# Kernel tuning notes

Hardware: AMD Instinct MI355X
Metric: run time of the kernel (lower is better)

The kernel has to match this reference:

```python
import jax, jax.numpy as jnp
import numpy as np

B, S, H = 2, 2048, 2048
NH, NKV, D = 32, 8, 64
GROUPS = NH // NKV
SCALE = D ** -0.5


def rotate_half(x):
    x1, x2 = x[..., : D // 2], x[..., D // 2 :]
    return jnp.concatenate((-x2, x1), axis=-1)


def setup_inputs() -> dict:
    key = jax.random.key(0)
    ks = jax.random.split(key, 8)
    x = jax.random.normal(ks[0], (B, S, H), dtype=jnp.float32)
    cos = jax.random.uniform(ks[1], (B, S, D), dtype=jnp.float32)
    sin = jax.random.uniform(ks[2], (B, S, D), dtype=jnp.float32)
    mask = jnp.tril(jnp.ones((S, S), dtype=jnp.int32))[None, None]  # causal (1,1,S,S)
    std = H ** -0.5
    wq = jax.random.normal(ks[3], (NH * D, H), dtype=jnp.float32) * std
    wk = jax.random.normal(ks[4], (NKV * D, H), dtype=jnp.float32) * std
    wv = jax.random.normal(ks[5], (NKV * D, H), dtype=jnp.float32) * std
    wo = jax.random.normal(ks[6], (H, NH * D), dtype=jnp.float32) * std
    return {"x": x, "cos": cos, "sin": sin, "mask": mask,
            "wq": wq, "wk": wk, "wv": wv, "wo": wo}


def reference(x, cos, sin, mask, wq, wk, wv, wo):
    b, s, _ = x.shape
    # projections (Linear: x @ W^T, no bias)
    q = (x @ wq.T).reshape(b, s, NH, D).transpose(0, 2, 1, 3)    # (b, nh, s, d)
    k = (x @ wk.T).reshape(b, s, NKV, D).transpose(0, 2, 1, 3)   # (b, nkv, s, d)
    v = (x @ wv.T).reshape(b, s, NKV, D).transpose(0, 2, 1, 3)
    # RoPE
    c = cos[:, None, :, :]
    sn = sin[:, None, :, :]
    q = q * c + rotate_half(q) * sn
    k = k * c + rotate_half(k) * sn
    # GQA: repeat KV heads
    k = jnp.repeat(k, GROUPS, axis=1)   # (b, nh, s, d)
    v = jnp.repeat(v, GROUPS, axis=1)
    scores = jnp.einsum("bhqd,bhkd->bhqk", q, k) * SCALE
    scores = jnp.where(mask == 0, -jnp.inf, scores)
    weights = jax.nn.softmax(scores, axis=-1)
    out = jnp.einsum("bhqk,bhkd->bhqd", weights, v)
    out = out.transpose(0, 2, 1, 3).reshape(b, s, NH * D)
    return out @ wo.T
```

## Files before the change

kernel.cpp:

```cpp
#include <hip/hip_runtime.h>
#include <hip/hip_bf16.h>
#include <math.h>

typedef __attribute__((ext_vector_type(8))) short bf16x8;
typedef __attribute__((ext_vector_type(4))) float f32x4;

__device__ __forceinline__ float bf2f(ushort u) {
  union { unsigned u; float f; } v; v.u = ((unsigned)u) << 16; return v.f;
}
__device__ __forceinline__ ushort f2bf(float f) {
  union { float f; unsigned u; } v; v.f = f;
  unsigned r = v.u + 0x7FFFu + ((v.u >> 16) & 1u);
  return (ushort)(r >> 16);
}
#if __has_builtin(__builtin_amdgcn_exp2f)
#define EXP2F(x) __builtin_amdgcn_exp2f(x)
#else
#define EXP2F(x) exp2f(x)
#endif
__device__ __forceinline__ void gl_lds16(const ushort* g, ushort* l) {
  __builtin_amdgcn_global_load_lds(
      (const __attribute__((address_space(1))) unsigned int*)g,
      (__attribute__((address_space(3))) unsigned int*)l, 16, 0, 0);
}

static const long XB   = 0;
static const long WQB  = 8388608;
static const long WKB  = 12582912;
static const long WVB  = 13631488;
static const long WOB  = 14680064;
static const long COSB = 18874368;
static const long SINB = 19136512;
static const long QB   = 19398656;
static const long KB   = 27787264;
static const long VTB  = 29884416;

__global__ void detect_dtype(const ushort* __restrict__ x, int* __restrict__ flag) {
  __shared__ int cnt;
  if (threadIdx.x == 0) cnt = 0;
  __syncthreads();
  int local = 0;
  for (int j = 0; j < 32; j++) {
    ushort u = x[threadIdx.x + j * 256];
    int e = (u >> 7) & 0xFF;
    if (e >= 100 && e <= 142) local++;
  }
  atomicAdd(&cnt, local);
  __syncthreads();
  if (threadIdx.x == 0) *flag = (cnt >= 6554) ? 1 : 0;
}

__global__ void cast_all(const void* __restrict__ s0, const void* __restrict__ s1,
                         const void* __restrict__ s2, const void* __restrict__ s3,
                         const void* __restrict__ s4, const void* __restrict__ s5,
                         const void* __restrict__ s6,
                         ushort* __restrict__ d0, ushort* __restrict__ d1,
                         ushort* __restrict__ d2, ushort* __restrict__ d3,
                         ushort* __restrict__ d4, ushort* __restrict__ d5,
                         ushort* __restrict__ d6, const int* __restrict__ flag) {
  if (*flag) return;
  const long N = 2424832;
  for (long i = (long)blockIdx.x * blockDim.x + threadIdx.x; i < N;
       i += (long)gridDim.x * blockDim.x) {
    const float4* s; ushort* d; long off;
    if      (i < 1048576) { s = (const float4*)s0; d = d0; off = i; }
    else if (i < 1572864) { s = (const float4*)s1; d = d1; off = i - 1048576; }
    else if (i < 1703936) { s = (const float4*)s2; d = d2; off = i - 1572864; }
    else if (i < 1835008) { s = (const float4*)s3; d = d3; off = i - 1703936; }
    else if (i < 2359296) { s = (const float4*)s4; d = d4; off = i - 1835008; }
    else if (i < 2392064) { s = (const float4*)s5; d = d5; off = i - 2359296; }
    else                  { s = (const float4*)s6; d = d6; off = i - 2392064; }
    float4 a = s[2 * off], b = s[2 * off + 1];
    uint4 o;
    o.x = (unsigned)f2bf(a.x) | ((unsigned)f2bf(a.y) << 16);
    o.y = (unsigned)f2bf(a.z) | ((unsigned)f2bf(a.w) << 16);
    o.z = (unsigned)f2bf(b.x) | ((unsigned)f2bf(b.y) << 16);
    o.w = (unsigned)f2bf(b.z) | ((unsigned)f2bf(b.w) << 16);
    ((uint4*)d)[off] = o;
  }
}

__device__ __forceinline__ void gemm_body(
    const ushort* __restrict__ A, const ushort* __restrict__ W, void* __restrict__ C,
    int N, int K, int bm, int bn, bool ofp32, ushort* As, ushort* Ws) {
  const int tid = threadIdx.x;
  const int wave = tid >> 6, lane = tid & 63;
  const int quad = lane >> 4, l15 = lane & 15;
  const int wm = (wave >> 1) * 64, wn = (wave & 1) * 64;
  const int srow = tid >> 2, sk = (tid & 3) * 8;
  const ushort* Ap = A + (size_t)(bm + srow) * K + sk;
  const ushort* Wp = W + (size_t)(bn + srow) * K + sk;
  ushort* AsW = As + wave * 512;
  ushort* WsW = Ws + wave * 512;
  f32x4 acc[4][4] = {};
  for (int k0 = 0; k0 < K; k0 += 32) {
    __syncthreads();
    gl_lds16(Ap + k0, AsW);
    gl_lds16(Ap + (size_t)64 * K + k0, AsW + 2048);
    gl_lds16(Wp + k0, WsW);
    gl_lds16(Wp + (size_t)64 * K + k0, WsW + 2048);
    __syncthreads();
    bf16x8 af[4], wf[4];
#pragma unroll
    for (int t = 0; t < 4; t++)
      af[t] = *(const bf16x8*)&As[(wm + t * 16 + l15) * 32 + quad * 8];
#pragma unroll
    for (int t = 0; t < 4; t++)
      wf[t] = *(const bf16x8*)&Ws[(wn + t * 16 + l15) * 32 + quad * 8];
#pragma unroll
    for (int mt = 0; mt < 4; mt++)
#pragma unroll
      for (int nt = 0; nt < 4; nt++)
        acc[mt][nt] = __builtin_amdgcn_mfma_f32_16x16x32_bf16(af[mt], wf[nt], acc[mt][nt], 0, 0, 0);
  }
  if (!ofp32) {
    ushort* Cb = (ushort*)C;
#pragma unroll
    for (int mt = 0; mt < 4; mt++)
#pragma unroll
      for (int nt = 0; nt < 4; nt++)
#pragma unroll
        for (int r = 0; r < 4; r++) {
          int row = bm + wm + mt * 16 + quad * 4 + r;
          int col = bn + wn + nt * 16 + l15;
          Cb[(size_t)row * N + col] = f2bf(acc[mt][nt][r]);
        }
  } else {
    float* Cf = (float*)C;
#pragma unroll
    for (int mt = 0; mt < 4; mt++)
#pragma unroll
      for (int nt = 0; nt < 4; nt++)
#pragma unroll
        for (int r = 0; r < 4; r++) {
          int row = bm + wm + mt * 16 + quad * 4 + r;
          int col = bn + wn + nt * 16 + l15;
          Cf[(size_t)row * N + col] = acc[mt][nt][r];
        }
  }
}

__global__ __launch_bounds__(256) void gemm_qkv(
    const ushort* __restrict__ xws, const ushort* __restrict__ xorig,
    const ushort* __restrict__ wqws, const ushort* __restrict__ wqorig,
    const ushort* __restrict__ wkws, const ushort* __restrict__ wkorig,
    const ushort* __restrict__ wvws, const ushort* __restrict__ wvorig,
    ushort* __restrict__ qout, ushort* __restrict__ kout, ushort* __restrict__ vtout,
    const int* __restrict__ flag) {
  __shared__ __align__(16) ushort As[128 * 32];
  __shared__ __align__(16) ushort Ws[128 * 32];
  const bool bf = (*flag != 0);
  const ushort* x = bf ? xorig : xws;
  const int id = blockIdx.x;
  if (id < 512) {
    gemm_body(x, bf ? wqorig : wqws, qout, 2048, 2048, (id >> 4) * 128, (id & 15) * 128, false, As, Ws);
  } else if (id < 640) {
    int t = id - 512;
    gemm_body(x, bf ? wkorig : wkws, kout, 512, 2048, (t >> 2) * 128, (t & 3) * 128, false, As, Ws);
  } else {
    int t = id - 640;
    gemm_body(bf ? wvorig : wvws, x, vtout, 4096, 2048, (t & 3) * 128, (t >> 2) * 128, false, As, Ws);
  }
}

__global__ __launch_bounds__(256) void gemm_bt(
    const ushort* __restrict__ Aws, const ushort* __restrict__ Aorig,
    const ushort* __restrict__ Wws, const ushort* __restrict__ Worig,
    void* __restrict__ C, int N, int K, const int* __restrict__ flag, int outMode) {
  __shared__ __align__(16) ushort As[128 * 32];
  __shared__ __align__(16) ushort Ws[128 * 32];
  const bool bf = (*flag != 0);
  const ushort* A = (bf && Aorig) ? Aorig : Aws;
  const ushort* W = (bf && Worig) ? Worig : Wws;
  bool ofp32 = (outMode == 1) && !bf;
  gemm_body(A, W, C, N, K, blockIdx.y * 128, blockIdx.x * 128, ofp32, As, Ws);
}

__global__ void rope_kernel(ushort* __restrict__ Qb, ushort* __restrict__ Kb,
                            const ushort* __restrict__ cws, const ushort* __restrict__ corig,
                            const ushort* __restrict__ sws, const ushort* __restrict__ sorig,
                            const int* __restrict__ flag) {
  const ushort* cb = (*flag) ? corig : cws;
  const ushort* sb = (*flag) ? sorig : sws;
  int i = blockIdx.x * 256 + threadIdx.x;
  ushort* base; long row; int c8; float scl;
  if (i < 524288) {
    row = i >> 7; int rest = i & 127; c8 = (rest & 3) * 8;
    base = Qb + row * 2048 + (rest >> 2) * 64 + c8;
    scl = 0.18033688011112f;
  } else {
    int j = i - 524288;
    row = j >> 5; int rest = j & 31; c8 = (rest & 3) * 8;
    base = Kb + row * 512 + (rest >> 2) * 64 + c8;
    scl = 1.0f;
  }
  uint4 lo4 = *(const uint4*)base;
  uint4 hi4 = *(const uint4*)(base + 32);
  uint4 cl4 = *(const uint4*)(cb + row * 64 + c8);
  uint4 ch4 = *(const uint4*)(cb + row * 64 + c8 + 32);
  uint4 sl4 = *(const uint4*)(sb + row * 64 + c8);
  uint4 sh4 = *(const uint4*)(sb + row * 64 + c8 + 32);
  const ushort* lo = (const ushort*)&lo4; const ushort* hi = (const ushort*)&hi4;
  const ushort* cl = (const ushort*)&cl4; const ushort* ch = (const ushort*)&ch4;
  const ushort* sl = (const ushort*)&sl4; const ushort* sh = (const ushort*)&sh4;
  uint4 olo, ohi;
  ushort* po = (ushort*)&olo; ushort* ph = (ushort*)&ohi;
#pragma unroll
  for (int k = 0; k < 8; k++) {
    float l = bf2f(lo[k]), h = bf2f(hi[k]);
    po[k] = f2bf((l * bf2f(cl[k]) - h * bf2f(sl[k])) * scl);
    ph[k] = f2bf((h * bf2f(ch[k]) + l * bf2f(sh[k])) * scl);
  }
  *(uint4*)base = olo;
  *(uint4*)(base + 32) = ohi;
}

__global__ __launch_bounds__(512, 4) void attn_kernel(
    const ushort* __restrict__ Qb, const ushort* __restrict__ Kb,
    const ushort* __restrict__ Vt, ushort* __restrict__ Ob) {
  __shared__ __align__(16) ushort Ks[2][4096];
  __shared__ __align__(16) ushort Vs[2][4096];
  __shared__ __align__(16) ushort Ps[128 * 72];
  const int tid = threadIdx.x;
  const int wave = tid >> 6, lane = tid & 63;
  const int quad = lane >> 4, l15 = lane & 15;
  const int id = blockIdx.x;
  const int kvh = id & 7;
  const int b = (id >> 3) & 1;
  const int hsub = (id >> 4) & 3;
  const int h = kvh * 4 + hsub;
  const int pr = id >> 6;
  const size_t brow = (size_t)b * 2048;
  const ushort* Kg = Kb + brow * 512 + (size_t)kvh * 64;
  const ushort* Vg = Vt + (size_t)(kvh * 64) * 4096 + brow;

  const int prow = wave * 16 + (lane >> 2);
  const int chunk = (lane & 3) * 8;
  const int k_s = prow & 63, k_kc = prow >> 6;
  const int v_d = prow & 63, v_sc = prow >> 6;
  const int ldsW = wave * 512;

  for (int ph = 0; ph < 2; ph++) {
    const int t = ph ? (15 - pr) : pr;
    const int q0 = t * 128;
    const int wrow0 = q0 + wave * 16;
    const int blockNt = 2 * t + 2;
    const int myLast = wrow0 >> 6;

    gl_lds16(Kg + (size_t)k_s * 512 + k_kc * 32 + chunk, &Ks[0][ldsW]);
    gl_lds16(Vg + (size_t)v_d * 4096 + v_sc * 32 + chunk, &Vs[0][ldsW]);

    bf16x8 qf[2];
#pragma unroll
    for (int kc = 0; kc < 2; kc++)
      qf[kc] = *(const bf16x8*)&Qb[(brow + wrow0 + l15) * 2048 + h * 64 + kc * 32 + quad * 8];

    float l_s[4] = {};
    f32x4 oacc[4] = {};

    __syncthreads();

    for (int nt = 0; nt < blockNt; nt++) {
      const int cur = nt & 1;
      if (nt + 1 < blockNt) {
        const int n1 = (nt + 1) * 64;
        gl_lds16(Kg + (size_t)(n1 + k_s) * 512 + k_kc * 32 + chunk, &Ks[cur ^ 1][ldsW]);
        gl_lds16(Vg + (size_t)v_d * 4096 + n1 + v_sc * 32 + chunk, &Vs[cur ^ 1][ldsW]);
      }
      if (nt <= myLast) {
        const int n0 = nt * 64;
        const ushort* Kc = Ks[cur];
        const ushort* Vc = Vs[cur];
        f32x4 sc[4];
        __builtin_amdgcn_s_setprio(1);
#pragma unroll
        for (int ct = 0; ct < 4; ct++) {
          bf16x8 kf0 = *(const bf16x8*)&Kc[(ct * 16 + l15) * 32 + quad * 8];
          bf16x8 kf1 = *(const bf16x8*)&Kc[2048 + (ct * 16 + l15) * 32 + quad * 8];
          f32x4 z = {0.f, 0.f, 0.f, 0.f};
          z = __builtin_amdgcn_mfma_f32_16x16x32_bf16(qf[0], kf0, z, 0, 0, 0);
          z = __builtin_amdgcn_mfma_f32_16x16x32_bf16(qf[1], kf1, z, 0, 0, 0);
          sc[ct] = z;
        }
        __builtin_amdgcn_s_setprio(0);
        const int rowb = wrow0 + quad * 4;
        if (nt == myLast) {
#pragma unroll
          for (int ct = 0; ct < 4; ct++)
#pragma unroll
            for (int r = 0; r < 4; r++)
              if (n0 + ct * 16 + l15 > rowb + r) sc[ct][r] = -INFINITY;
        }
#pragma unroll
        for (int ct = 0; ct < 4; ct++)
#pragma unroll
          for (int r = 0; r < 4; r++) {
            float pv = EXP2F(sc[ct][r] - 23.083120654223f);
            l_s[r] += pv;
            Ps[(wave * 16 + quad * 4 + r) * 72 + ct * 16 + l15] =
                (ushort)((__float_as_uint(pv) + 0x8000u) >> 16);
          }
        bf16x8 pf0 = *(const bf16x8*)&Ps[(wave * 16 + l15) * 72 + quad * 8];
        bf16x8 pf1 = *(const bf16x8*)&Ps[(wave * 16 + l15) * 72 + 32 + quad * 8];
        __builtin_amdgcn_s_setprio(1);
#pragma unroll
        for (int dt = 0; dt < 4; dt++) {
          bf16x8 vf0 = *(const bf16x8*)&Vc[(dt * 16 + l15) * 32 + quad * 8];
          bf16x8 vf1 = *(const bf16x8*)&Vc[2048 + (dt * 16 + l15) * 32 + quad * 8];
          oacc[dt] = __builtin_amdgcn_mfma_f32_16x16x32_bf16(pf0, vf0, oacc[dt], 0, 0, 0);
          oacc[dt] = __builtin_amdgcn_mfma_f32_16x16x32_bf16(pf1, vf1, oacc[dt], 0, 0, 0);
        }
        __builtin_amdgcn_s_setprio(0);
      }
      __syncthreads();
    }
#pragma unroll
    for (int r = 0; r < 4; r++) {
      float l = l_s[r];
#pragma unroll
      for (int off = 1; off < 16; off <<= 1) l += __shfl_xor(l, off, 64);
      l_s[r] = 1.f / l;
    }
#pragma unroll
    for (int dt = 0; dt < 4; dt++)
#pragma unroll
      for (int r = 0; r < 4; r++) {
        int s = wrow0 + quad * 4 + r;
        Ob[(brow + s) * 2048 + h * 64 + dt * 16 + l15] = f2bf(oacc[dt][r] * l_s[r]);
      }
  }
}

extern "C" void kernel_launch(void* const* d_in, const int* in_sizes, int n_in,
                              void* d_out, int out_size, void* d_ws, size_t ws_size,
                              hipStream_t stream) {
  char* wsb = (char*)d_ws;
  int* flag = (int*)wsb;
  ushort* base = (ushort*)(wsb + 256);
  ushort* xb   = base + XB;
  ushort* wqb  = base + WQB;
  ushort* wkb  = base + WKB;
  ushort* wvb  = base + WVB;
  ushort* wob  = base + WOB;
  ushort* cosb = base + COSB;
  ushort* sinb = base + SINB;
  ushort* qb   = base + QB;
  ushort* kb   = base + KB;
  ushort* vtb  = base + VTB;
  ushort* abuf = xb;

  const ushort* xo  = (const ushort*)d_in[0];
  const ushort* co  = (const ushort*)d_in[1];
  const ushort* so  = (const ushort*)d_in[2];
  const ushort* wqo = (const ushort*)d_in[4];
  const ushort* wko = (const ushort*)d_in[5];
  const ushort* wvo = (const ushort*)d_in[6];
  const ushort* woo = (const ushort*)d_in[7];

  detect_dtype<<<1, 256, 0, stream>>>(xo, flag);

  cast_all<<<4096, 256, 0, stream>>>(d_in[0], d_in[4], d_in[5], d_in[6], d_in[7],
                                     d_in[1], d_in[2],
                                     xb, wqb, wkb, wvb, wob, cosb, sinb, flag);

  gemm_qkv<<<768, 256, 0, stream>>>(xb, xo, wqb, wqo, wkb, wko, wvb, wvo,
                                    qb, kb, vtb, flag);

  rope_kernel<<<2560, 256, 0, stream>>>(qb, kb, cosb, co, sinb, so, flag);

  attn_kernel<<<512, 512, 0, stream>>>(qb, kb, vtb, abuf);

  gemm_bt<<<dim3(16, 32), 256, 0, stream>>>(abuf, nullptr, wob, woo, d_out, 2048, 2048, flag, 1);
}
```

Before: 317.3 us.

## Fuse RoPE into QKV GEMM epilogue and split attention into one tile per block

RoPE is now applied in the QKV GEMM epilogue, pairing accumulator columns nt and nt^2 inside each 64-wide head tile, so the separate rope kernel and its extra read-modify-write pass over Q and K go away. The attention kernel stops looping over two paired query tiles per block. It launches 1024 blocks, each handling one tile, largest first. The QK MFMA operands are swapped so scores come out transposed, which lets P be written to LDS as packed 32-bit pairs and the row sum be reduced with fewer shuffles. The epilogue now does strided cos/sin loads, and per-block causal work is no longer balanced by pairing tiles.

```diff
diff --git a/kernel.cpp b/kernel.cpp
--- a/kernel.cpp
+++ b/kernel.cpp
@@ -82,7 +82,8 @@
 
 __device__ __forceinline__ void gemm_body(
     const ushort* __restrict__ A, const ushort* __restrict__ W, void* __restrict__ C,
-    int N, int K, int bm, int bn, bool ofp32, ushort* As, ushort* Ws) {
+    int N, int K, int bm, int bn, bool ofp32, ushort* As, ushort* Ws,
+    int ropeMode, const ushort* __restrict__ cosp, const ushort* __restrict__ sinp) {
   const int tid = threadIdx.x;
   const int wave = tid >> 6, lane = tid & 63;
   const int quad = lane >> 4, l15 = lane & 15;
@@ -113,7 +114,28 @@
       for (int nt = 0; nt < 4; nt++)
         acc[mt][nt] = __builtin_amdgcn_mfma_f32_16x16x32_bf16(af[mt], wf[nt], acc[mt][nt], 0, 0, 0);
   }
-  if (!ofp32) {
+  if (ropeMode) {
+    ushort* Cb = (ushort*)C;
+    const float scl = (ropeMode == 1) ? 0.18033688011112f : 1.0f;
+#pragma unroll
+    for (int mt = 0; mt < 4; mt++)
+#pragma unroll
+      for (int r = 0; r < 4; r++) {
+        int row = bm + wm + mt * 16 + quad * 4 + r;
+        const ushort* crow = cosp + (size_t)row * 64;
+        const ushort* srw  = sinp + (size_t)row * 64;
+#pragma unroll
+        for (int nt = 0; nt < 4; nt++) {
+          int d = nt * 16 + l15;
+          float a = acc[mt][nt][r];
+          float p = acc[mt][nt ^ 2][r];
+          float cs = bf2f(crow[d]), sn = bf2f(srw[d]);
+          float o = (nt < 2) ? (a * cs - p * sn) : (a * cs + p * sn);
+          int col = bn + wn + nt * 16 + l15;
+          Cb[(size_t)row * N + col] = f2bf(o * scl);
+        }
+      }
+  } else if (!ofp32) {
     ushort* Cb = (ushort*)C;
 #pragma unroll
     for (int mt = 0; mt < 4; mt++)
@@ -145,21 +167,28 @@
     const ushort* __restrict__ wqws, const ushort* __restrict__ wqorig,
     const ushort* __restrict__ wkws, const ushort* __restrict__ wkorig,
     const ushort* __restrict__ wvws, const ushort* __restrict__ wvorig,
+    const ushort* __restrict__ cws, const ushort* __restrict__ corig,
+    const ushort* __restrict__ sws, const ushort* __restrict__ sorig,
     ushort* __restrict__ qout, ushort* __restrict__ kout, ushort* __restrict__ vtout,
     const int* __restrict__ flag) {
   __shared__ __align__(16) ushort As[128 * 32];
   __shared__ __align__(16) ushort Ws[128 * 32];
   const bool bf = (*flag != 0);
   const ushort* x = bf ? xorig : xws;
+  const ushort* cp = bf ? corig : cws;
+  const ushort* sp = bf ? sorig : sws;
   const int id = blockIdx.x;
   if (id < 512) {
-    gemm_body(x, bf ? wqorig : wqws, qout, 2048, 2048, (id >> 4) * 128, (id & 15) * 128, false, As, Ws);
+    gemm_body(x, bf ? wqorig : wqws, qout, 2048, 2048, (id >> 4) * 128, (id & 15) * 128,
+              false, As, Ws, 1, cp, sp);
   } else if (id < 640) {
     int t = id - 512;
-    gemm_body(x, bf ? wkorig : wkws, kout, 512, 2048, (t >> 2) * 128, (t & 3) * 128, false, As, Ws);
+    gemm_body(x, bf ? wkorig : wkws, kout, 512, 2048, (t >> 2) * 128, (t & 3) * 128,
+              false, As, Ws, 2, cp, sp);
   } else {
     int t = id - 640;
-    gemm_body(bf ? wvorig : wvws, x, vtout, 4096, 2048, (t & 3) * 128, (t >> 2) * 128, false, As, Ws);
+    gemm_body(bf ? wvorig : wvws, x, vtout, 4096, 2048, (t & 3) * 128, (t >> 2) * 128,
+              false, As, Ws, 0, nullptr, nullptr);
   }
 }
 
@@ -173,46 +202,8 @@
   const ushort* A = (bf && Aorig) ? Aorig : Aws;
   const ushort* W = (bf && Worig) ? Worig : Wws;
   bool ofp32 = (outMode == 1) && !bf;
-  gemm_body(A, W, C, N, K, blockIdx.y * 128, blockIdx.x * 128, ofp32, As, Ws);
-}
-
-__global__ void rope_kernel(ushort* __restrict__ Qb, ushort* __restrict__ Kb,
-                            const ushort* __restrict__ cws, const ushort* __restrict__ corig,
-                            const ushort* __restrict__ sws, const ushort* __restrict__ sorig,
-                            const int* __restrict__ flag) {
-  const ushort* cb = (*flag) ? corig : cws;
-  const ushort* sb = (*flag) ? sorig : sws;
-  int i = blockIdx.x * 256 + threadIdx.x;
-  ushort* base; long row; int c8; float scl;
-  if (i < 524288) {
-    row = i >> 7; int rest = i & 127; c8 = (rest & 3) * 8;
-    base = Qb + row * 2048 + (rest >> 2) * 64 + c8;
-    scl = 0.18033688011112f;
-  } else {
-    int j = i - 524288;
-    row = j >> 5; int rest = j & 31; c8 = (rest & 3) * 8;
-    base = Kb + row * 512 + (rest >> 2) * 64 + c8;
-    scl = 1.0f;
-  }
-  uint4 lo4 = *(const uint4*)base;
-  uint4 hi4 = *(const uint4*)(base + 32);
-  uint4 cl4 = *(const uint4*)(cb + row * 64 + c8);
-  uint4 ch4 = *(const uint4*)(cb + row * 64 + c8 + 32);
-  uint4 sl4 = *(const uint4*)(sb + row * 64 + c8);
-  uint4 sh4 = *(const uint4*)(sb + row * 64 + c8 + 32);
-  const ushort* lo = (const ushort*)&lo4; const ushort* hi = (const ushort*)&hi4;
-  const ushort* cl = (const ushort*)&cl4; const ushort* ch = (const ushort*)&ch4;
-  const ushort* sl = (const ushort*)&sl4; const ushort* sh = (const ushort*)&sh4;
-  uint4 olo, ohi;
-  ushort* po = (ushort*)&olo; ushort* ph = (ushort*)&ohi;
-#pragma unroll
-  for (int k = 0; k < 8; k++) {
-    float l = bf2f(lo[k]), h = bf2f(hi[k]);
-    po[k] = f2bf((l * bf2f(cl[k]) - h * bf2f(sl[k])) * scl);
-    ph[k] = f2bf((h * bf2f(ch[k]) + l * bf2f(sh[k])) * scl);
-  }
-  *(uint4*)base = olo;
-  *(uint4*)(base + 32) = ohi;
+  gemm_body(A, W, C, N, K, blockIdx.y * 128, blockIdx.x * 128, ofp32, As, Ws,
+            0, nullptr, nullptr);
 }
 
 __global__ __launch_bounds__(512, 4) void attn_kernel(
@@ -229,7 +220,7 @@
   const int b = (id >> 3) & 1;
   const int hsub = (id >> 4) & 3;
   const int h = kvh * 4 + hsub;
-  const int pr = id >> 6;
+  const int t = 15 - (id >> 6);
   const size_t brow = (size_t)b * 2048;
   const ushort* Kg = Kb + brow * 512 + (size_t)kvh * 64;
   const ushort* Vg = Vt + (size_t)(kvh * 64) * 4096 + brow;
@@ -240,95 +231,92 @@
   const int v_d = prow & 63, v_sc = prow >> 6;
   const int ldsW = wave * 512;
 
-  for (int ph = 0; ph < 2; ph++) {
-    const int t = ph ? (15 - pr) : pr;
-    const int q0 = t * 128;
-    const int wrow0 = q0 + wave * 16;
-    const int blockNt = 2 * t + 2;
-    const int myLast = wrow0 >> 6;
-
-    gl_lds16(Kg + (size_t)k_s * 512 + k_kc * 32 + chunk, &Ks[0][ldsW]);
-    gl_lds16(Vg + (size_t)v_d * 4096 + v_sc * 32 + chunk, &Vs[0][ldsW]);
-
-    bf16x8 qf[2];
-#pragma unroll
-    for (int kc = 0; kc < 2; kc++)
-      qf[kc] = *(const bf16x8*)&Qb[(brow + wrow0 + l15) * 2048 + h * 64 + kc * 32 + quad * 8];
-
-    float l_s[4] = {};
-    f32x4 oacc[4] = {};
-
+  const int q0 = t * 128;
+  const int wrow0 = q0 + wave * 16;
+  const int blockNt = 2 * t + 2;
+  const int myLast = wrow0 >> 6;
+
+  gl_lds16(Kg + (size_t)k_s * 512 + k_kc * 32 + chunk, &Ks[0][ldsW]);
+  gl_lds16(Vg + (size_t)v_d * 4096 + v_sc * 32 + chunk, &Vs[0][ldsW]);
+
+  bf16x8 qf[2];
+#pragma unroll
+  for (int kc = 0; kc < 2; kc++)
+    qf[kc] = *(const bf16x8*)&Qb[(brow + wrow0 + l15) * 2048 + h * 64 + kc * 32 + quad * 8];
+
+  float l_loc = 0.f;
+  f32x4 oacc[4] = {};
+
+  __syncthreads();
+
+  for (int nt = 0; nt < blockNt; nt++) {
+    const int cur = nt & 1;
+    if (nt + 1 < blockNt) {
+      const int n1 = (nt + 1) * 64;
+      gl_lds16(Kg + (size_t)(n1 + k_s) * 512 + k_kc * 32 + chunk, &Ks[cur ^ 1][ldsW]);
+      gl_lds16(Vg + (size_t)v_d * 4096 + n1 + v_sc * 32 + chunk, &Vs[cur ^ 1][ldsW]);
+    }
+    if (nt <= myLast) {
+      const int n0 = nt * 64;
+      const ushort* Kc = Ks[cur];
+      const ushort* Vc = Vs[cur];
+      f32x4 sc[4];
+      __builtin_amdgcn_s_setprio(1);
+#pragma unroll
+      for (int ct = 0; ct < 4; ct++) {
+        bf16x8 kf0 = *(const bf16x8*)&Kc[(ct * 16 + l15) * 32 + quad * 8];
+        bf16x8 kf1 = *(const bf16x8*)&Kc[2048 + (ct * 16 + l15) * 32 + quad * 8];
+        f32x4 z = {0.f, 0.f, 0.f, 0.f};
+        z = __builtin_amdgcn_mfma_f32_16x16x32_bf16(kf0, qf[0], z, 0, 0, 0);
+        z = __builtin_amdgcn_mfma_f32_16x16x32_bf16(kf1, qf[1], z, 0, 0, 0);
+        sc[ct] = z;
+      }
+      __builtin_amdgcn_s_setprio(0);
+      if (nt == myLast) {
+        const int qrow = wrow0 + l15;
+#pragma unroll
+        for (int ct = 0; ct < 4; ct++)
+#pragma unroll
+          for (int r = 0; r < 4; r++)
+            if (n0 + ct * 16 + quad * 4 + r > qrow) sc[ct][r] = -INFINITY;
+      }
+#pragma unroll
+      for (int ct = 0; ct < 4; ct++)
+#pragma unroll
+        for (int k = 0; k < 2; k++) {
+          float pv0 = EXP2F(sc[ct][2 * k]     - 23.083120654223f);
+          float pv1 = EXP2F(sc[ct][2 * k + 1] - 23.083120654223f);
+          l_loc += pv0 + pv1;
+          unsigned u = ((__float_as_uint(pv0) + 0x8000u) >> 16) |
+                       ((__float_as_uint(pv1) + 0x8000u) & 0xFFFF0000u);
+          *(unsigned*)&Ps[(wave * 16 + l15) * 72 + ct * 16 + quad * 4 + 2 * k] = u;
+        }
+      bf16x8 pf0 = *(const bf16x8*)&Ps[(wave * 16 + l15) * 72 + quad * 8];
+      bf16x8 pf1 = *(const bf16x8*)&Ps[(wave * 16 + l15) * 72 + 32 + quad * 8];
+      __builtin_amdgcn_s_setprio(1);
+#pragma unroll
+      for (int dt = 0; dt < 4; dt++) {
+        bf16x8 vf0 = *(const bf16x8*)&Vc[(dt * 16 + l15) * 32 + quad * 8];
+        bf16x8 vf1 = *(const bf16x8*)&Vc[2048 + (dt * 16 + l15) * 32 + quad * 8];
+        oacc[dt] = __builtin_amdgcn_mfma_f32_16x16x32_bf16(pf0, vf0, oacc[dt], 0, 0, 0);
+        oacc[dt] = __builtin_amdgcn_mfma_f32_16x16x32_bf16(pf1, vf1, oacc[dt], 0, 0, 0);
+      }
+      __builtin_amdgcn_s_setprio(0);
+    }
     __syncthreads();
-
-    for (int nt = 0; nt < blockNt; nt++) {
-      const int cur = nt & 1;
-      if (nt + 1 < blockNt) {
-        const int n1 = (nt + 1) * 64;
-        gl_lds16(Kg + (size_t)(n1 + k_s) * 512 + k_kc * 32 + chunk, &Ks[cur ^ 1][ldsW]);
-        gl_lds16(Vg + (size_t)v_d * 4096 + n1 + v_sc * 32 + chunk, &Vs[cur ^ 1][ldsW]);
-      }
-      if (nt <= myLast) {
-        const int n0 = nt * 64;
-        const ushort* Kc = Ks[cur];
-        const ushort* Vc = Vs[cur];
-        f32x4 sc[4];
-        __builtin_amdgcn_s_setprio(1);
-#pragma unroll
-        for (int ct = 0; ct < 4; ct++) {
-          bf16x8 kf0 = *(const bf16x8*)&Kc[(ct * 16 + l15) * 32 + quad * 8];
-          bf16x8 kf1 = *(const bf16x8*)&Kc[2048 + (ct * 16 + l15) * 32 + quad * 8];
-          f32x4 z = {0.f, 0.f, 0.f, 0.f};
-          z = __builtin_amdgcn_mfma_f32_16x16x32_bf16(qf[0], kf0, z, 0, 0, 0);
-          z = __builtin_amdgcn_mfma_f32_16x16x32_bf16(qf[1], kf1, z, 0, 0, 0);
-          sc[ct] = z;
-        }
-        __builtin_amdgcn_s_setprio(0);
-        const int rowb = wrow0 + quad * 4;
-        if (nt == myLast) {
-#pragma unroll
-          for (int ct = 0; ct < 4; ct++)
-#pragma unroll
-            for (int r = 0; r < 4; r++)
-              if (n0 + ct * 16 + l15 > rowb + r) sc[ct][r] = -INFINITY;
-        }
-#pragma unroll
-        for (int ct = 0; ct < 4; ct++)
-#pragma unroll
-          for (int r = 0; r < 4; r++) {
-            float pv = EXP2F(sc[ct][r] - 23.083120654223f);
-            l_s[r] += pv;
-            Ps[(wave * 16 + quad * 4 + r) * 72 + ct * 16 + l15] =
-                (ushort)((__float_as_uint(pv) + 0x8000u) >> 16);
-          }
-        bf16x8 pf0 = *(const bf16x8*)&Ps[(wave * 16 + l15) * 72 + quad * 8];
-        bf16x8 pf1 = *(const bf16x8*)&Ps[(wave * 16 + l15) * 72 + 32 + quad * 8];
-        __builtin_amdgcn_s_setprio(1);
-#pragma unroll
-        for (int dt = 0; dt < 4; dt++) {
-          bf16x8 vf0 = *(const bf16x8*)&Vc[(dt * 16 + l15) * 32 + quad * 8];
-          bf16x8 vf1 = *(const bf16x8*)&Vc[2048 + (dt * 16 + l15) * 32 + quad * 8];
-          oacc[dt] = __builtin_amdgcn_mfma_f32_16x16x32_bf16(pf0, vf0, oacc[dt], 0, 0, 0);
-          oacc[dt] = __builtin_amdgcn_mfma_f32_16x16x32_bf16(pf1, vf1, oacc[dt], 0, 0, 0);
-        }
-        __builtin_amdgcn_s_setprio(0);
-      }
-      __syncthreads();
+  }
+  l_loc += __shfl_xor(l_loc, 16, 64);
+  l_loc += __shfl_xor(l_loc, 32, 64);
+  float linv[4];
+#pragma unroll
+  for (int r = 0; r < 4; r++) linv[r] = 1.f / __shfl(l_loc, quad * 4 + r, 64);
+#pragma unroll
+  for (int dt = 0; dt < 4; dt++)
+#pragma unroll
+    for (int r = 0; r < 4; r++) {
+      int s = wrow0 + quad * 4 + r;
+      Ob[(brow + s) * 2048 + h * 64 + dt * 16 + l15] = f2bf(oacc[dt][r] * linv[r]);
     }
-#pragma unroll
-    for (int r = 0; r < 4; r++) {
-      float l = l_s[r];
-#pragma unroll
-      for (int off = 1; off < 16; off <<= 1) l += __shfl_xor(l, off, 64);
-      l_s[r] = 1.f / l;
-    }
-#pragma unroll
-    for (int dt = 0; dt < 4; dt++)
-#pragma unroll
-      for (int r = 0; r < 4; r++) {
-        int s = wrow0 + quad * 4 + r;
-        Ob[(brow + s) * 2048 + h * 64 + dt * 16 + l15] = f2bf(oacc[dt][r] * l_s[r]);
-      }
-  }
 }
 
 extern "C" void kernel_launch(void* const* d_in, const int* in_sizes, int n_in,
@@ -364,11 +352,9 @@
                                      xb, wqb, wkb, wvb, wob, cosb, sinb, flag);
 
   gemm_qkv<<<768, 256, 0, stream>>>(xb, xo, wqb, wqo, wkb, wko, wvb, wvo,
-                                    qb, kb, vtb, flag);
-
-  rope_kernel<<<2560, 256, 0, stream>>>(qb, kb, cosb, co, sinb, so, flag);
-
-  attn_kernel<<<512, 512, 0, stream>>>(qb, kb, vtb, abuf);
+                                    cosb, co, sinb, so, qb, kb, vtb, flag);
+
+  attn_kernel<<<1024, 512, 0, stream>>>(qb, kb, vtb, abuf);
 
   gemm_bt<<<dim3(16, 32), 256, 0, stream>>>(abuf, nullptr, wob, woo, d_out, 2048, 2048, flag, 1);
 }
```

Measured after the change: 334.7 us. +5.5%, slower.
